# Kernel tuning notes

Hardware: AMD Instinct MI355X
Metric: run time of the kernel (lower is better)

The kernel has to match this reference:

```python
import jax, jax.numpy as jnp
import numpy as np

WS = 16          # window_size
OWS = 24         # overlap_win_size = int(ws*0.5) + ws
PAD = (OWS - WS) // 2
NH = 6           # num_heads


def _ln(x, g, b):
    m = jnp.mean(x, axis=-1, keepdims=True)
    v = jnp.mean((x - m) ** 2, axis=-1, keepdims=True)
    return (x - m) * jax.lax.rsqrt(v + 1e-5) * g + b


def setup_inputs() -> dict:
    key = jax.random.key(0)
    ks = jax.random.split(key, 12)
    B, H, W, C = 4, 64, 64, 180
    std = 0.02
    x = jax.random.normal(ks[0], (B, H * W, C), jnp.float32)
    y = jax.random.normal(ks[1], (B, H * W, C), jnp.float32)
    kv_w = jax.random.normal(ks[2], (2 * C, C), jnp.float32) * std
    kv_b = jnp.zeros((2 * C,), jnp.float32)
    q_w = jax.random.normal(ks[3], (C, C), jnp.float32) * std
    q_b = jnp.zeros((C,), jnp.float32)
    rpb = jax.random.normal(ks[4], ((WS + OWS - 1) ** 2, NH), jnp.float32) * std
    proj_w = jax.random.normal(ks[5], (C, C), jnp.float32) * std
    proj_b = jnp.zeros((C,), jnp.float32)
    fc1_w = jax.random.normal(ks[6], (4 * C, C), jnp.float32) * std
    fc1_b = jnp.zeros((4 * C,), jnp.float32)
    fc2_w = jax.random.normal(ks[7], (C, 4 * C), jnp.float32) * std
    fc2_b = jnp.zeros((C,), jnp.float32)
    norm1_g = jnp.ones((C,), jnp.float32); norm1_b = jnp.zeros((C,), jnp.float32)
    norm2_g = jnp.ones((C,), jnp.float32); norm2_b = jnp.zeros((C,), jnp.float32)
    # relative position index (HAT-style OCA): query coords vs extended window coords
    co = np.stack(np.meshgrid(np.arange(WS), np.arange(WS), indexing='ij')).reshape(2, -1)   # 2, ws*ws
    ce = np.stack(np.meshgrid(np.arange(OWS), np.arange(OWS), indexing='ij')).reshape(2, -1) # 2, ows*ows
    rel = (ce[:, None, :] - co[:, :, None]).transpose(1, 2, 0) + (WS - 1)  # nq, n, 2 in [0, ws+ows-2]
    rpi = jnp.asarray(rel[..., 0] * (WS + OWS - 1) + rel[..., 1], jnp.int32)  # [256, 576]
    return {
        'x': x, 'y': y,
        'norm1_g': norm1_g, 'norm1_b': norm1_b,
        'kv_w': kv_w, 'kv_b': kv_b, 'q_w': q_w, 'q_b': q_b,
        'rpb': rpb, 'proj_w': proj_w, 'proj_b': proj_b,
        'norm2_g': norm2_g, 'norm2_b': norm2_b,
        'fc1_w': fc1_w, 'fc1_b': fc1_b, 'fc2_w': fc2_w, 'fc2_b': fc2_b,
        'rpi': rpi, 'h': 64, 'w': 64,
    }


def reference(x, y, norm1_g, norm1_b, kv_w, kv_b, q_w, q_b, rpb, proj_w, proj_b,
              norm2_g, norm2_b, fc1_w, fc1_b, fc2_w, fc2_b, rpi, h, w):
    b, L, c = x.shape
    nh = NH
    d = c // nh
    scale = d ** -0.5
    nwh, nww = h // WS, w // WS
    nq, n = WS * WS, OWS * OWS

    shortcut = x
    xn = _ln(x, norm1_g, norm1_b).reshape(b, h, w, c)
    yn = _ln(y, norm1_g, norm1_b).reshape(b, h, w, c)

    kv = xn @ kv_w.T + kv_b                                  # b,h,w,2c
    q = yn @ q_w.T + q_b                                     # b,h,w,c

    # kv -> [2, b, c, h, w] then pad spatially and extract overlapping windows (nn.Unfold)
    kv = kv.reshape(b, h, w, 2, c).transpose(3, 0, 4, 1, 2)  # 2,b,c,h,w
    kvp = jnp.pad(kv, ((0, 0), (0, 0), (0, 0), (PAD, PAD), (PAD, PAD)))
    hh = jnp.arange(nwh)[:, None] * WS + jnp.arange(OWS)[None, :]   # [nwh, OWS]
    ww = jnp.arange(nww)[:, None] * WS + jnp.arange(OWS)[None, :]   # [nww, OWS]
    patches = kvp[:, :, :, hh][:, :, :, :, :, ww]            # 2,b,c,nwh,OWS,nww,OWS
    kvw = patches.transpose(0, 1, 3, 5, 4, 6, 2).reshape(2, b * nwh * nww, n, c)
    kwin, vwin = kvw[0], kvw[1]                              # [b_, n, c]

    # non-overlapping query windows (window_partition)
    qwin = q.reshape(b, nwh, WS, nww, WS, c).transpose(0, 1, 3, 2, 4, 5).reshape(-1, nq, c)
    b_ = qwin.shape[0]

    qh = qwin.reshape(b_, nq, nh, d).transpose(0, 2, 1, 3) * scale
    kh = kwin.reshape(b_, n, nh, d).transpose(0, 2, 1, 3)
    vh = vwin.reshape(b_, n, nh, d).transpose(0, 2, 1, 3)

    attn = jnp.einsum('bhqd,bhkd->bhqk', qh, kh)             # [b_, nh, nq, n]
    bias = rpb[rpi.reshape(-1)].reshape(nq, n, nh).transpose(2, 0, 1)  # [nh, nq, n]
    attn = jax.nn.softmax(attn + bias[None], axis=-1)
    out = jnp.einsum('bhqk,bhkd->bhqd', attn, vh).transpose(0, 2, 1, 3).reshape(b_, nq, c)

    # window_reverse
    out = out.reshape(b, nwh, nww, WS, WS, c).transpose(0, 1, 3, 2, 4, 5).reshape(b, h * w, c)

    xo = out @ proj_w.T + proj_b + shortcut
    xn2 = _ln(xo, norm2_g, norm2_b)
    mlp = jax.nn.gelu(xn2 @ fc1_w.T + fc1_b, approximate=False) @ fc2_w.T + fc2_b
    return xo + mlp
```

## Files before the change

kernel.cpp:

```cpp
#include <hip/hip_runtime.h>

typedef __bf16 bf16;
typedef __bf16 bf16x8 __attribute__((ext_vector_type(8)));
typedef __bf16 bf16x4 __attribute__((ext_vector_type(4)));
typedef __bf16 bf16x2 __attribute__((ext_vector_type(2)));
typedef float f32x4 __attribute__((ext_vector_type(4)));

static __device__ __forceinline__ bf16x8 ld8(const bf16* p) {
    return *reinterpret_cast<const bf16x8*>(p);
}
static __device__ __forceinline__ bf16x4 ld4(const bf16* p) {
    return *reinterpret_cast<const bf16x4*>(p);
}
static __device__ __forceinline__ bf16x8 ld8_b32(const bf16* p) {
    bf16x8 v;
#pragma unroll
    for (int i = 0; i < 4; ++i) {
        bf16x2 t = *reinterpret_cast<const bf16x2*>(p + i * 2);
        v[i * 2] = t[0]; v[i * 2 + 1] = t[1];
    }
    return v;
}
static __device__ __forceinline__ bf16x8 zero8() {
    bf16x8 v;
#pragma unroll
    for (int i = 0; i < 8; ++i) v[i] = (bf16)0.f;
    return v;
}

#define MFMA16(a, b, c) __builtin_amdgcn_mfma_f32_16x16x32_bf16((a), (b), (c), 0, 0, 0)

template <int ROWS, int BK, int KPAD, int THREADS>
static __device__ __forceinline__ void load_chunk_g(const bf16* __restrict__ g,
                                                    bf16x8* r, int tid) {
    constexpr int TOT = ROWS * BK / 8;
    constexpr int NP = (TOT + THREADS - 1) / THREADS;
#pragma unroll
    for (int p = 0; p < NP; ++p) {
        int idx = p * THREADS + tid;
        if ((TOT % THREADS) == 0 || idx < TOT) {
            int row = idx / (BK / 8), cg = idx % (BK / 8);
            r[p] = ld8(g + (long)row * KPAD + cg * 8);
        }
    }
}
template <int ROWS, int BK, int THREADS>
static __device__ __forceinline__ void store_chunk_l(bf16* __restrict__ lds,
                                                     const bf16x8* r, int tid) {
    constexpr int TOT = ROWS * BK / 8;
    constexpr int NP = (TOT + THREADS - 1) / THREADS;
#pragma unroll
    for (int p = 0; p < NP; ++p) {
        int idx = p * THREADS + tid;
        if ((TOT % THREADS) == 0 || idx < TOT) {
            int row = idx / (BK / 8), cg = idx % (BK / 8);
            *reinterpret_cast<bf16x8*>(lds + row * 200 + cg * 8) = r[p];
        }
    }
}
template <int ROWS, int BK, int KPAD, int THREADS>
static __device__ __forceinline__ void stage_tile(const bf16* __restrict__ g,
                                                  bf16* __restrict__ lds, int tid) {
    constexpr int TOT = ROWS * BK / 8;
    constexpr int NP = (TOT + THREADS - 1) / THREADS;
#pragma unroll
    for (int p = 0; p < NP; ++p) {
        int idx = p * THREADS + tid;
        if ((TOT % THREADS) == 0 || idx < TOT) {
            int row = idx / (BK / 8), cg = idx % (BK / 8);
            bf16x8 v = ld8(g + (long)row * KPAD + cg * 8);
            *reinterpret_cast<bf16x8*>(lds + row * 200 + cg * 8) = v;
        }
    }
}

__global__ __launch_bounds__(256) void fused_pre(
    const float* __restrict__ x, const float* __restrict__ y,
    const float* __restrict__ g, const float* __restrict__ b,
    bf16* __restrict__ dst,
    const float* __restrict__ kv_w, const float* __restrict__ q_w,
    const float* __restrict__ proj_w, const float* __restrict__ fc1_w,
    const float* __restrict__ fc2_w, const float* __restrict__ rpb,
    const int* __restrict__ rpi,
    bf16* __restrict__ wkv, bf16* __restrict__ wq, bf16* __restrict__ wproj,
    bf16* __restrict__ wfc1, bf16* __restrict__ wfc2, bf16* __restrict__ biast)
{
    if (blockIdx.x < 8192) {
        int wave = threadIdx.x >> 6, lane = threadIdx.x & 63;
        int row = blockIdx.x * 4 + wave;
        const float* sp = (row < 16384) ? (x + (long)row * 180)
                                        : (y + (long)(row - 16384) * 180);
        float v0 = sp[lane];
        float v1 = sp[lane + 64];
        float v2 = (lane < 52) ? sp[lane + 128] : 0.f;
        float s = v0 + v1 + v2;
        float sq = v0 * v0 + v1 * v1 + v2 * v2;
#pragma unroll
        for (int m = 32; m >= 1; m >>= 1) {
            s += __shfl_xor(s, m);
            sq += __shfl_xor(sq, m);
        }
        float mean = s * (1.f / 180.f);
        float var = sq * (1.f / 180.f) - mean * mean;
        float rs = rsqrtf(var + 1e-5f);
        bf16* dp = dst + (long)row * 192;
        dp[lane] = (bf16)((v0 - mean) * rs * g[lane] + b[lane]);
        dp[lane + 64] = (bf16)((v1 - mean) * rs * g[lane + 64] + b[lane + 64]);
        float o2 = (lane < 52) ? ((v2 - mean) * rs * g[lane + 128] + b[lane + 128]) : 0.f;
        dp[lane + 128] = (bf16)o2;
        return;
    }
    int i = (blockIdx.x - 8192) * 256 + threadIdx.x;
    if (i < 73728) {
        int n = i / 192, k = i % 192;
        float v = (n < 360 && k < 180) ? kv_w[n * 180 + k] : 0.f;
        wkv[i] = (bf16)v;
    } else if (i < 122880) {
        int j = i - 73728; int n = j / 192, k = j % 192;
        float v = (n < 180 && k < 180) ? q_w[n * 180 + k] : 0.f;
        wq[j] = (bf16)v;
    } else if (i < 172032) {
        int j = i - 122880; int n = j / 192, k = j % 192;
        int hh = k >> 5, d = k & 31;
        float v = (n < 180 && d < 30) ? proj_w[n * 180 + hh * 30 + d] : 0.f;
        wproj[j] = (bf16)v;
    } else if (i < 319488) {
        int j = i - 172032; int n = j / 192, k = j % 192;
        float v = (n < 720 && k < 180) ? fc1_w[n * 180 + k] : 0.f;
        wfc1[j] = (bf16)v;
    } else if (i < 507904) {
        int j = i - 319488; int n = j / 736, k = j % 736;
        float v = (n < 180 && k < 720) ? fc2_w[n * 720 + k] : 0.f;
        wfc2[j] = (bf16)v;
    } else if (i < 1392640) {
        int t = i - 507904;
        int r = t & 3;
        int lane = (t >> 2) & 63;
        int tmp2 = t >> 8;
        int kg = tmp2 % 36;
        int tmp3 = tmp2 / 36;
        int qg = tmp3 & 15;
        int h = tmp3 >> 4;
        int q = qg * 16 + (lane & 15);
        int key = kg * 16 + ((lane >> 4) << 2) + r;
        biast[t] = (bf16)rpb[rpi[q * 576 + key] * 6 + h];
    }
}

__global__ __launch_bounds__(512, 4) void gemm_kvq(
    const bf16* __restrict__ xn, const bf16* __restrict__ yn,
    const bf16* __restrict__ wkv, const bf16* __restrict__ wq,
    const float* __restrict__ kv_b, const float* __restrict__ q_b,
    bf16* __restrict__ kvbuf, bf16* __restrict__ qbuf)
{
    const int tid = threadIdx.x, wave = tid >> 6, lane = tid & 63;
    const int llo = lane & 15, quad = lane >> 4;
    const int bz = blockIdx.y;
    const bool isq = (bz == 2);
    const bf16* A = isq ? yn : xn;
    const bf16* Wbase = isq ? wq : (wkv + (long)bz * 3 * 64 * 192);
    const int tm = blockIdx.x * 128;

    __shared__ __align__(16) bf16 Sa[128 * 200];
    __shared__ __align__(16) bf16 Sb[64 * 200];

    stage_tile<128, 192, 192, 512>(A + (long)tm * 192, Sa, tid);
    bf16x8 wreg[3];
    load_chunk_g<64, 192, 192, 512>(Wbase, wreg, tid);

    for (int s = 0; s < 3; ++s) {
        if (s) __syncthreads();
        store_chunk_l<64, 192, 512>(Sb, wreg, tid);
        __syncthreads();
        if (s < 2) load_chunk_g<64, 192, 192, 512>(Wbase + (long)(s + 1) * 64 * 192, wreg, tid);

        f32x4 acc[4];
#pragma unroll
        for (int nt = 0; nt < 4; ++nt)
#pragma unroll
            for (int r = 0; r < 4; ++r) acc[nt][r] = 0.f;
#pragma unroll
        for (int kt = 0; kt < 6; ++kt) {
            bf16x8 a = ld8(Sa + (wave * 16 + llo) * 200 + kt * 32 + quad * 8);
#pragma unroll
            for (int nt = 0; nt < 4; ++nt) {
                bf16x8 b = ld8(Sb + (nt * 16 + llo) * 200 + kt * 32 + quad * 8);
                acc[nt] = MFMA16(a, b, acc[nt]);
            }
        }

        const int g = bz * 3 + s;
#pragma unroll
        for (int nt = 0; nt < 4; ++nt) {
            int n = g * 64 + nt * 16 + llo;
            if (!isq) {
                if (n < 360) {
                    int nn = n % 180;
                    int col = (n / 180) * 192 + (nn / 30) * 32 + (nn % 30);
                    float bv = kv_b[n];
#pragma unroll
                    for (int r = 0; r < 4; ++r) {
                        int m = tm + wave * 16 + quad * 4 + r;
                        kvbuf[(long)m * 384 + col] = (bf16)(acc[nt][r] + bv);
                    }
                }
            } else {
                int nq = n - 384;
                if (nq < 180) {
                    int col = (nq / 30) * 32 + (nq % 30);
                    float bv = q_b[nq];
#pragma unroll
                    for (int r = 0; r < 4; ++r) {
                        int m = tm + wave * 16 + quad * 4 + r;
                        qbuf[(long)m * 192 + col] =
                            (bf16)((acc[nt][r] + bv) * 0.18257418583505537f);
                    }
                }
            }
        }
    }
}

__global__ __launch_bounds__(512, 6) void attn_kernel(
    const bf16* __restrict__ qbuf, const bf16* __restrict__ kvbuf,
    const bf16* __restrict__ biast, bf16* __restrict__ obuf)
{
    const int qhalf = blockIdx.x & 1;
    const int head = (blockIdx.x >> 1) % 6;
    const int win = blockIdx.x / 12;
    const int bb = win / 16, wi = (win % 16) / 4, wj = win % 4;
    const int tid = threadIdx.x;
    const int wave = tid >> 6, lane = tid & 63;
    const int llo = lane & 15, quad = lane >> 4;
    const int qbase = qhalf * 128 + wave * 16;
    const int qg = qhalf * 8 + wave;

    __shared__ bf16 Kc[2][64][40];
    __shared__ bf16 Vt[2][32][74];
    __shared__ bf16 Ps[8][16][72];

    const int u = tid & 255;
    const int tloc = u >> 2, dq = u & 3;
    const bool isV = tid >= 256;
    int aa = tloc / 24, w0 = tloc % 24;

    const int q0 = qbase + llo;
    const int gr_q = bb * 4096 + (wi * 16 + (q0 >> 4)) * 64 + (wj * 16 + (q0 & 15));
    const bf16x8 qf = ld8(qbuf + (long)gr_q * 192 + head * 32 + quad * 8);
    const bf16* bbase = biast + ((long)(head * 16 + qg) * 36) * 256 + lane * 4;

    {
        int gy = wi * 16 + aa - 4, gx = wj * 16 + w0 - 4;
        bf16x8 st = zero8();
        if ((unsigned)gy < 64u && (unsigned)gx < 64u) {
            long gr = (long)(bb * 4096 + gy * 64 + gx) * 384;
            st = ld8(kvbuf + gr + (isV ? 192 : 0) + head * 32 + dq * 8);
        }
        if (!isV) {
            *reinterpret_cast<bf16x8*>(&Kc[0][tloc][dq * 8]) = st;
        } else {
#pragma unroll
            for (int j = 0; j < 8; ++j) Vt[0][dq * 8 + j][tloc] = st[j];
        }
    }
    __syncthreads();

    f32x4 o[2];
    float m_run = -1e30f, l_run = 0.f;
#pragma unroll
    for (int n2 = 0; n2 < 2; ++n2)
#pragma unroll
        for (int r = 0; r < 4; ++r) o[n2][r] = 0.f;

    for (int c = 0; c < 9; ++c) {
        const int cur = c & 1;

        bf16x8 stage;
        if (c < 8) {
            w0 += 16; aa += 2;
            if (w0 >= 24) { w0 -= 24; ++aa; }
            int gy = wi * 16 + aa - 4, gx = wj * 16 + w0 - 4;
            stage = zero8();
            if ((unsigned)gy < 64u && (unsigned)gx < 64u) {
                long gr = (long)(bb * 4096 + gy * 64 + gx) * 384;
                stage = ld8(kvbuf + gr + (isV ? 192 : 0) + head * 32 + dq * 8);
            }
        }

        f32x4 s[4];
#pragma unroll
        for (int kt = 0; kt < 4; ++kt) {
            bf16x8 kf = ld8(&Kc[cur][kt * 16 + llo][quad * 8]);
            f32x4 zc;
            zc[0] = 0.f; zc[1] = 0.f; zc[2] = 0.f; zc[3] = 0.f;
            s[kt] = MFMA16(kf, qf, zc);
        }

#pragma unroll
        for (int kt = 0; kt < 4; ++kt) {
            bf16x4 bv = ld4(bbase + (c * 4 + kt) * 256);
#pragma unroll
            for (int r = 0; r < 4; ++r) s[kt][r] += (float)bv[r];
        }

        float mx = s[0][0];
#pragma unroll
        for (int kt = 0; kt < 4; ++kt)
#pragma unroll
            for (int r = 0; r < 4; ++r) mx = fmaxf(mx, s[kt][r]);
        mx = fmaxf(mx, __shfl_xor(mx, 16));
        mx = fmaxf(mx, __shfl_xor(mx, 32));
        float m_new = fmaxf(m_run, mx);
        float alpha = __expf(m_run - m_new);
        float ls = 0.f;
#pragma unroll
        for (int kt = 0; kt < 4; ++kt)
#pragma unroll
            for (int r = 0; r < 4; ++r) {
                float p = __expf(s[kt][r] - m_new);
                s[kt][r] = p;
                ls += p;
            }
        ls += __shfl_xor(ls, 16);
        ls += __shfl_xor(ls, 32);
        l_run = l_run * alpha + ls;
        m_run = m_new;

#pragma unroll
        for (int r = 0; r < 4; ++r) {
            float a = __shfl(alpha, quad * 4 + r);
            o[0][r] *= a;
            o[1][r] *= a;
        }

#pragma unroll
        for (int kt = 0; kt < 4; ++kt) {
            bf16x4 pv;
#pragma unroll
            for (int r = 0; r < 4; ++r) pv[r] = (bf16)s[kt][r];
            *reinterpret_cast<bf16x4*>(&Ps[wave][llo][kt * 16 + quad * 4]) = pv;
        }

#pragma unroll
        for (int kt2 = 0; kt2 < 2; ++kt2) {
            bf16x8 pa = ld8(&Ps[wave][llo][kt2 * 32 + quad * 8]);
#pragma unroll
            for (int n2 = 0; n2 < 2; ++n2) {
                bf16x8 vb = ld8_b32(&Vt[cur][n2 * 16 + llo][kt2 * 32 + quad * 8]);
                o[n2] = MFMA16(pa, vb, o[n2]);
            }
        }

        if (c < 8) {
            if (!isV) {
                *reinterpret_cast<bf16x8*>(&Kc[1 - cur][tloc][dq * 8]) = stage;
            } else {
#pragma unroll
                for (int j = 0; j < 8; ++j) Vt[1 - cur][dq * 8 + j][tloc] = stage[j];
            }
            __syncthreads();
        }
    }

    float linv = 1.f / l_run;
#pragma unroll
    for (int r = 0; r < 4; ++r) {
        float li = __shfl(linv, quad * 4 + r);
        int q = qbase + quad * 4 + r;
        int gr = bb * 4096 + (wi * 16 + (q >> 4)) * 64 + (wj * 16 + (q & 15));
#pragma unroll
        for (int n2 = 0; n2 < 2; ++n2)
            obuf[(long)gr * 192 + head * 32 + n2 * 16 + llo] = (bf16)(o[n2][r] * li);
    }
}

__global__ __launch_bounds__(256, 3) void gemm_projln(
    const bf16* __restrict__ obuf, const bf16* __restrict__ wproj,
    const float* __restrict__ proj_b, const float* __restrict__ x,
    const float* __restrict__ g, const float* __restrict__ bln,
    float* __restrict__ xo, bf16* __restrict__ xn2)
{
    const int tid = threadIdx.x, wave = tid >> 6, lane = tid & 63;
    const int llo = lane & 15, quad = lane >> 4;
    const int mbase = blockIdx.x * 64;

    __shared__ __align__(16) bf16 Sa[64 * 200];
    __shared__ __align__(16) bf16 Sb[64 * 200];
    stage_tile<64, 192, 192, 256>(obuf + (long)mbase * 192, Sa, tid);
    bf16x8 wreg[6];
    load_chunk_g<64, 192, 192, 256>(wproj, wreg, tid);

    f32x4 acc[12];
#pragma unroll
    for (int nt = 0; nt < 12; ++nt)
#pragma unroll
        for (int r = 0; r < 4; ++r) acc[nt][r] = 0.f;

    for (int nc = 0; nc < 3; ++nc) {
        if (nc) __syncthreads();
        store_chunk_l<64, 192, 256>(Sb, wreg, tid);
        __syncthreads();
        if (nc < 2) load_chunk_g<64, 192, 192, 256>(wproj + (long)(nc + 1) * 64 * 192, wreg, tid);
#pragma unroll
        for (int kt = 0; kt < 6; ++kt) {
            bf16x8 a = ld8(Sa + (wave * 16 + llo) * 200 + kt * 32 + quad * 8);
#pragma unroll
            for (int nt = 0; nt < 4; ++nt) {
                bf16x8 b = ld8(Sb + (nt * 16 + llo) * 200 + kt * 32 + quad * 8);
                acc[nc * 4 + nt] = MFMA16(a, b, acc[nc * 4 + nt]);
            }
        }
    }

#pragma unroll
    for (int r = 0; r < 4; ++r) {
        int m = mbase + wave * 16 + quad * 4 + r;
        float v[12];
        float sum = 0.f, sq = 0.f;
#pragma unroll
        for (int nt = 0; nt < 12; ++nt) {
            int n = nt * 16 + llo;
            float val = 0.f;
            if (n < 180) val = acc[nt][r] + proj_b[n] + x[(long)m * 180 + n];
            v[nt] = val;
            sum += val; sq += val * val;
        }
#pragma unroll
        for (int msk = 1; msk <= 8; msk <<= 1) {
            sum += __shfl_xor(sum, msk);
            sq  += __shfl_xor(sq, msk);
        }
        float mean = sum * (1.f / 180.f);
        float var = sq * (1.f / 180.f) - mean * mean;
        float rs = rsqrtf(var + 1e-5f);
#pragma unroll
        for (int nt = 0; nt < 12; ++nt) {
            int n = nt * 16 + llo;
            if (n < 180) {
                xo[(long)m * 180 + n] = v[nt];
                xn2[(long)m * 192 + n] = (bf16)((v[nt] - mean) * rs * g[n] + bln[n]);
            } else {
                xn2[(long)m * 192 + n] = (bf16)0.f;
            }
        }
    }
}

__global__ __launch_bounds__(512, 4) void gemm_fc1(
    const bf16* __restrict__ A, const bf16* __restrict__ W,
    const float* __restrict__ bias, bf16* __restrict__ outp)
{
    const int tid = threadIdx.x, wave = tid >> 6, lane = tid & 63;
    const int llo = lane & 15, quad = lane >> 4;
    const int tm = blockIdx.x * 128;
    const int bz = blockIdx.y;
    const bf16* Wbase = W + (long)bz * 3 * 64 * 192;

    __shared__ __align__(16) bf16 Sa[128 * 200];
    __shared__ __align__(16) bf16 Sb[64 * 200];
    stage_tile<128, 192, 192, 512>(A + (long)tm * 192, Sa, tid);
    bf16x8 wreg[3];
    load_chunk_g<64, 192, 192, 512>(Wbase, wreg, tid);

    for (int s = 0; s < 3; ++s) {
        if (s) __syncthreads();
        store_chunk_l<64, 192, 512>(Sb, wreg, tid);
        __syncthreads();
        if (s < 2) load_chunk_g<64, 192, 192, 512>(Wbase + (long)(s + 1) * 64 * 192, wreg, tid);

        f32x4 acc[4];
#pragma unroll
        for (int nt = 0; nt < 4; ++nt)
#pragma unroll
            for (int r = 0; r < 4; ++r) acc[nt][r] = 0.f;
#pragma unroll
        for (int kt = 0; kt < 6; ++kt) {
            bf16x8 a = ld8(Sa + (wave * 16 + llo) * 200 + kt * 32 + quad * 8);
#pragma unroll
            for (int nt = 0; nt < 4; ++nt) {
                bf16x8 b = ld8(Sb + (nt * 16 + llo) * 200 + kt * 32 + quad * 8);
                acc[nt] = MFMA16(a, b, acc[nt]);
            }
        }

        const int nb = (bz * 3 + s) * 64;
#pragma unroll
        for (int nt = 0; nt < 4; ++nt) {
            int n = nb + nt * 16 + llo;
            if (n >= 720) continue;
            float bv = bias[n];
#pragma unroll
            for (int r = 0; r < 4; ++r) {
                int m = tm + wave * 16 + quad * 4 + r;
                float v = acc[nt][r] + bv;
                float gel = 0.5f * v * (1.f + erff(v * 0.7071067811865475f));
                outp[(long)m * 736 + n] = (bf16)gel;
            }
        }
    }
}

__global__ __launch_bounds__(256, 4) void gemm_fc2(
    const bf16* __restrict__ A, const bf16* __restrict__ W,
    const float* __restrict__ bias, const float* __restrict__ resid,
    float* __restrict__ outp)
{
    const int tid = threadIdx.x, wave = tid >> 6, lane = tid & 63;
    const int llo = lane & 15, quad = lane >> 4;
    const int tm = blockIdx.x * 64;
    const int tn = blockIdx.y * 64;

    __shared__ __align__(16) bf16 Sa[64 * 200];
    __shared__ __align__(16) bf16 Sb[64 * 200];

    const bf16* Ap = A + (long)tm * 736;
    const bf16* Wp = W + (long)tn * 736;

    bf16x8 ar[6], wr[6];
    load_chunk_g<64, 192, 736, 256>(Ap, ar, tid);
    load_chunk_g<64, 192, 736, 256>(Wp, wr, tid);

    f32x4 acc[4];
#pragma unroll
    for (int nt = 0; nt < 4; ++nt)
#pragma unroll
        for (int r = 0; r < 4; ++r) acc[nt][r] = 0.f;

#pragma unroll
    for (int c = 0; c < 4; ++c) {
        if (c) __syncthreads();
        if (c < 3) {
            store_chunk_l<64, 192, 256>(Sa, ar, tid);
            store_chunk_l<64, 192, 256>(Sb, wr, tid);
        } else {
            store_chunk_l<64, 160, 256>(Sa, ar, tid);
            store_chunk_l<64, 160, 256>(Sb, wr, tid);
        }
        __syncthreads();
        if (c < 2) {
            load_chunk_g<64, 192, 736, 256>(Ap + (c + 1) * 192, ar, tid);
            load_chunk_g<64, 192, 736, 256>(Wp + (c + 1) * 192, wr, tid);
        } else if (c == 2) {
            load_chunk_g<64, 160, 736, 256>(Ap + 576, ar, tid);
            load_chunk_g<64, 160, 736, 256>(Wp + 576, wr, tid);
        }
        const int nkt = (c == 3) ? 5 : 6;
        for (int kt = 0; kt < nkt; ++kt) {
            bf16x8 a = ld8(Sa + (wave * 16 + llo) * 200 + kt * 32 + quad * 8);
#pragma unroll
            for (int nt = 0; nt < 4; ++nt) {
                bf16x8 b = ld8(Sb + (nt * 16 + llo) * 200 + kt * 32 + quad * 8);
                acc[nt] = MFMA16(a, b, acc[nt]);
            }
        }
    }

#pragma unroll
    for (int nt = 0; nt < 4; ++nt)
#pragma unroll
        for (int r = 0; r < 4; ++r) {
            int m = tm + wave * 16 + quad * 4 + r;
            int n = tn + nt * 16 + llo;
            if (n >= 180) continue;
            float v = acc[nt][r] + bias[n];
            outp[(long)m * 180 + n] = v + resid[(long)m * 180 + n];
        }
}

extern "C" void kernel_launch(void* const* d_in, const int* in_sizes, int n_in,
                              void* d_out, int out_size, void* d_ws, size_t ws_size,
                              hipStream_t stream) {
    const float* x      = (const float*)d_in[0];
    const float* y      = (const float*)d_in[1];
    const float* n1g    = (const float*)d_in[2];
    const float* n1b    = (const float*)d_in[3];
    const float* kv_w   = (const float*)d_in[4];
    const float* kv_b   = (const float*)d_in[5];
    const float* q_w    = (const float*)d_in[6];
    const float* q_b    = (const float*)d_in[7];
    const float* rpb    = (const float*)d_in[8];
    const float* proj_w = (const float*)d_in[9];
    const float* proj_b = (const float*)d_in[10];
    const float* n2g    = (const float*)d_in[11];
    const float* n2b    = (const float*)d_in[12];
    const float* fc1_w  = (const float*)d_in[13];
    const float* fc1_b  = (const float*)d_in[14];
    const float* fc2_w  = (const float*)d_in[15];
    const float* fc2_b  = (const float*)d_in[16];
    const int*   rpi    = (const int*)d_in[17];

    char* ws = (char*)d_ws;
    bf16* xn    = (bf16*)(ws + 0);
    bf16* yn    = (bf16*)(ws + 6291456);
    bf16* qbuf  = (bf16*)(ws + 12582912);
    bf16* kvbuf = (bf16*)(ws + 18874368);
    bf16* obuf  = (bf16*)(ws + 31457280);
    float* xo   = (float*)(ws + 37748736);
    bf16* biast = (bf16*)(ws + 49545216);
    bf16* wkv   = (bf16*)(ws + 51314688);
    bf16* wq    = (bf16*)(ws + 51462144);
    bf16* wproj = (bf16*)(ws + 51560448);
    bf16* wfc1  = (bf16*)(ws + 51658752);
    bf16* wfc2  = (bf16*)(ws + 51953664);
    bf16* hmid  = (bf16*)(ws + 6291456);
    bf16* xn2   = xn;

    fused_pre<<<13632, 256, 0, stream>>>(x, y, n1g, n1b, xn,
                                         kv_w, q_w, proj_w, fc1_w, fc2_w, rpb, rpi,
                                         wkv, wq, wproj, wfc1, wfc2, biast);
    gemm_kvq<<<dim3(128, 3), 512, 0, stream>>>(xn, yn, wkv, wq, kv_b, q_b, kvbuf, qbuf);
    attn_kernel<<<768, 512, 0, stream>>>(qbuf, kvbuf, biast, obuf);
    gemm_projln<<<256, 256, 0, stream>>>(obuf, wproj, proj_b, x, n2g, n2b, xo, xn2);
    gemm_fc1<<<dim3(128, 4), 512, 0, stream>>>(xn2, wfc1, fc1_b, hmid);
    gemm_fc2<<<dim3(256, 3), 256, 0, stream>>>(hmid, wfc2, fc2_b, xo, (float*)d_out);
}
```

Baseline: 200.0 us.

## Merge all stages into one persistent kernel with grid-wide barriers

Replaces the six separate kernel launches with a single persistent kernel of 256 blocks. The stages (layernorm plus weight prep, KV/Q GEMM, windowed attention, projection plus layernorm, fc1, fc2) are separated by atomic grid barriers. Work is redistributed over a fixed block count with per-block loops, and the barrier counters are reset each call with a memset. This removes launch gaps and tail effects between stages. In exchange, occupancy is limited to 256 blocks, which may leave the GPU's compute units underused, and the barriers spin-wait and assume every block is co-resident.

```diff
diff --git a/kernel.cpp b/kernel.cpp
--- a/kernel.cpp
+++ b/kernel.cpp
@@ -74,497 +74,523 @@
     }
 }
 
-__global__ __launch_bounds__(256) void fused_pre(
+#define NBLK 256u
+
+static __device__ __forceinline__ void gridbar(unsigned* bar) {
+    __threadfence();
+    __syncthreads();
+    if (threadIdx.x == 0) {
+        __hip_atomic_fetch_add(bar, 1u, __ATOMIC_ACQ_REL, __HIP_MEMORY_SCOPE_AGENT);
+        while (__hip_atomic_load(bar, __ATOMIC_ACQUIRE, __HIP_MEMORY_SCOPE_AGENT) < NBLK)
+            __builtin_amdgcn_s_sleep(2);
+    }
+    __syncthreads();
+    __threadfence();
+}
+
+__global__ __launch_bounds__(512, 2) void mega(
     const float* __restrict__ x, const float* __restrict__ y,
-    const float* __restrict__ g, const float* __restrict__ b,
-    bf16* __restrict__ dst,
-    const float* __restrict__ kv_w, const float* __restrict__ q_w,
-    const float* __restrict__ proj_w, const float* __restrict__ fc1_w,
-    const float* __restrict__ fc2_w, const float* __restrict__ rpb,
-    const int* __restrict__ rpi,
-    bf16* __restrict__ wkv, bf16* __restrict__ wq, bf16* __restrict__ wproj,
-    bf16* __restrict__ wfc1, bf16* __restrict__ wfc2, bf16* __restrict__ biast)
+    const float* __restrict__ n1g, const float* __restrict__ n1b,
+    const float* __restrict__ kv_w, const float* __restrict__ kv_b,
+    const float* __restrict__ q_w, const float* __restrict__ q_b,
+    const float* __restrict__ rpb, const int* __restrict__ rpi,
+    const float* __restrict__ proj_w, const float* __restrict__ proj_b,
+    const float* __restrict__ n2g, const float* __restrict__ n2b,
+    const float* __restrict__ fc1_w, const float* __restrict__ fc1_b,
+    const float* __restrict__ fc2_w, const float* __restrict__ fc2_b,
+    bf16* __restrict__ xn, bf16* __restrict__ yn,
+    bf16* __restrict__ qbuf, bf16* __restrict__ kvbuf,
+    bf16* __restrict__ obuf, float* __restrict__ xo,
+    bf16* __restrict__ biast, bf16* __restrict__ wkv, bf16* __restrict__ wq,
+    bf16* __restrict__ wproj, bf16* __restrict__ wfc1, bf16* __restrict__ wfc2,
+    bf16* __restrict__ hmid, bf16* __restrict__ xn2,
+    float* __restrict__ outp, unsigned* __restrict__ bars)
 {
-    if (blockIdx.x < 8192) {
-        int wave = threadIdx.x >> 6, lane = threadIdx.x & 63;
-        int row = blockIdx.x * 4 + wave;
-        const float* sp = (row < 16384) ? (x + (long)row * 180)
-                                        : (y + (long)(row - 16384) * 180);
-        float v0 = sp[lane];
-        float v1 = sp[lane + 64];
-        float v2 = (lane < 52) ? sp[lane + 128] : 0.f;
-        float s = v0 + v1 + v2;
-        float sq = v0 * v0 + v1 * v1 + v2 * v2;
-#pragma unroll
-        for (int m = 32; m >= 1; m >>= 1) {
-            s += __shfl_xor(s, m);
-            sq += __shfl_xor(sq, m);
-        }
-        float mean = s * (1.f / 180.f);
-        float var = sq * (1.f / 180.f) - mean * mean;
-        float rs = rsqrtf(var + 1e-5f);
-        bf16* dp = dst + (long)row * 192;
-        dp[lane] = (bf16)((v0 - mean) * rs * g[lane] + b[lane]);
-        dp[lane + 64] = (bf16)((v1 - mean) * rs * g[lane + 64] + b[lane + 64]);
-        float o2 = (lane < 52) ? ((v2 - mean) * rs * g[lane + 128] + b[lane + 128]) : 0.f;
-        dp[lane + 128] = (bf16)o2;
-        return;
-    }
-    int i = (blockIdx.x - 8192) * 256 + threadIdx.x;
-    if (i < 73728) {
-        int n = i / 192, k = i % 192;
-        float v = (n < 360 && k < 180) ? kv_w[n * 180 + k] : 0.f;
-        wkv[i] = (bf16)v;
-    } else if (i < 122880) {
-        int j = i - 73728; int n = j / 192, k = j % 192;
-        float v = (n < 180 && k < 180) ? q_w[n * 180 + k] : 0.f;
-        wq[j] = (bf16)v;
-    } else if (i < 172032) {
-        int j = i - 122880; int n = j / 192, k = j % 192;
-        int hh = k >> 5, d = k & 31;
-        float v = (n < 180 && d < 30) ? proj_w[n * 180 + hh * 30 + d] : 0.f;
-        wproj[j] = (bf16)v;
-    } else if (i < 319488) {
-        int j = i - 172032; int n = j / 192, k = j % 192;
-        float v = (n < 720 && k < 180) ? fc1_w[n * 180 + k] : 0.f;
-        wfc1[j] = (bf16)v;
-    } else if (i < 507904) {
-        int j = i - 319488; int n = j / 736, k = j % 736;
-        float v = (n < 180 && k < 720) ? fc2_w[n * 720 + k] : 0.f;
-        wfc2[j] = (bf16)v;
-    } else if (i < 1392640) {
-        int t = i - 507904;
-        int r = t & 3;
-        int lane = (t >> 2) & 63;
-        int tmp2 = t >> 8;
-        int kg = tmp2 % 36;
-        int tmp3 = tmp2 / 36;
-        int qg = tmp3 & 15;
-        int h = tmp3 >> 4;
-        int q = qg * 16 + (lane & 15);
-        int key = kg * 16 + ((lane >> 4) << 2) + r;
-        biast[t] = (bf16)rpb[rpi[q * 576 + key] * 6 + h];
-    }
-}
-
-__global__ __launch_bounds__(512, 4) void gemm_kvq(
-    const bf16* __restrict__ xn, const bf16* __restrict__ yn,
-    const bf16* __restrict__ wkv, const bf16* __restrict__ wq,
-    const float* __restrict__ kv_b, const float* __restrict__ q_b,
-    bf16* __restrict__ kvbuf, bf16* __restrict__ qbuf)
-{
-    const int tid = threadIdx.x, wave = tid >> 6, lane = tid & 63;
+    __shared__ __align__(16) char SM[76800];
+    const int tid = threadIdx.x;
+    const int blk = blockIdx.x;
+    const int wave = tid >> 6, lane = tid & 63;
     const int llo = lane & 15, quad = lane >> 4;
-    const int bz = blockIdx.y;
-    const bool isq = (bz == 2);
-    const bf16* A = isq ? yn : xn;
-    const bf16* Wbase = isq ? wq : (wkv + (long)bz * 3 * 64 * 192);
-    const int tm = blockIdx.x * 128;
-
-    __shared__ __align__(16) bf16 Sa[128 * 200];
-    __shared__ __align__(16) bf16 Sb[64 * 200];
-
-    stage_tile<128, 192, 192, 512>(A + (long)tm * 192, Sa, tid);
-    bf16x8 wreg[3];
-    load_chunk_g<64, 192, 192, 512>(Wbase, wreg, tid);
-
-    for (int s = 0; s < 3; ++s) {
-        if (s) __syncthreads();
-        store_chunk_l<64, 192, 512>(Sb, wreg, tid);
+
+    {
+#pragma unroll 2
+        for (int it = 0; it < 16; ++it) {
+            int row = blk * 128 + it * 8 + wave;
+            const float* sp = (row < 16384) ? (x + (long)row * 180)
+                                            : (y + (long)(row - 16384) * 180);
+            float v0 = sp[lane];
+            float v1 = sp[lane + 64];
+            float v2 = (lane < 52) ? sp[lane + 128] : 0.f;
+            float s = v0 + v1 + v2;
+            float sq = v0 * v0 + v1 * v1 + v2 * v2;
+#pragma unroll
+            for (int m = 32; m >= 1; m >>= 1) {
+                s += __shfl_xor(s, m);
+                sq += __shfl_xor(sq, m);
+            }
+            float mean = s * (1.f / 180.f);
+            float var = sq * (1.f / 180.f) - mean * mean;
+            float rs = rsqrtf(var + 1e-5f);
+            bf16* dp = ((row < 16384) ? xn : (yn - 16384 * 192)) + (long)row * 192;
+            dp[lane] = (bf16)((v0 - mean) * rs * n1g[lane] + n1b[lane]);
+            dp[lane + 64] = (bf16)((v1 - mean) * rs * n1g[lane + 64] + n1b[lane + 64]);
+            float o2 = (lane < 52) ? ((v2 - mean) * rs * n1g[lane + 128] + n1b[lane + 128]) : 0.f;
+            dp[lane + 128] = (bf16)o2;
+        }
+        for (int i = blk * 512 + tid; i < 1392640; i += 131072) {
+            if (i < 73728) {
+                int n = i / 192, k = i % 192;
+                float v = (n < 360 && k < 180) ? kv_w[n * 180 + k] : 0.f;
+                wkv[i] = (bf16)v;
+            } else if (i < 122880) {
+                int j = i - 73728; int n = j / 192, k = j % 192;
+                float v = (n < 180 && k < 180) ? q_w[n * 180 + k] : 0.f;
+                wq[j] = (bf16)v;
+            } else if (i < 172032) {
+                int j = i - 122880; int n = j / 192, k = j % 192;
+                int hh = k >> 5, d = k & 31;
+                float v = (n < 180 && d < 30) ? proj_w[n * 180 + hh * 30 + d] : 0.f;
+                wproj[j] = (bf16)v;
+            } else if (i < 319488) {
+                int j = i - 172032; int n = j / 192, k = j % 192;
+                float v = (n < 720 && k < 180) ? fc1_w[n * 180 + k] : 0.f;
+                wfc1[j] = (bf16)v;
+            } else if (i < 507904) {
+                int j = i - 319488; int n = j / 736, k = j % 736;
+                float v = (n < 180 && k < 720) ? fc2_w[n * 720 + k] : 0.f;
+                wfc2[j] = (bf16)v;
+            } else {
+                int t = i - 507904;
+                int r = t & 3;
+                int ln = (t >> 2) & 63;
+                int tmp2 = t >> 8;
+                int kg = tmp2 % 36;
+                int tmp3 = tmp2 / 36;
+                int qg = tmp3 & 15;
+                int h = tmp3 >> 4;
+                int q = qg * 16 + (ln & 15);
+                int key = kg * 16 + ((ln >> 4) << 2) + r;
+                biast[t] = (bf16)rpb[rpi[q * 576 + key] * 6 + h];
+            }
+        }
+    }
+    gridbar(bars + 0);
+
+    {
+        bf16* Sa = (bf16*)SM;
+        bf16* Sb = (bf16*)(SM + 51200);
+        const int tmi = blk >> 1;
+        const int tm = tmi * 128;
+        const bool oddb = blk & 1;
+        const bf16* A = oddb ? yn : xn;
+        stage_tile<128, 192, 192, 512>(A + (long)tm * 192, Sa, tid);
+        const int nbz = oddb ? 1 : 2;
+        for (int zz = 0; zz < nbz; ++zz) {
+            const int bz = oddb ? 2 : zz;
+            const bool isq = (bz == 2);
+            const bf16* Wbase = isq ? wq : (wkv + (long)bz * 3 * 64 * 192);
+            bf16x8 wreg[3];
+            load_chunk_g<64, 192, 192, 512>(Wbase, wreg, tid);
+            for (int s = 0; s < 3; ++s) {
+                if (s || zz) __syncthreads();
+                store_chunk_l<64, 192, 512>(Sb, wreg, tid);
+                __syncthreads();
+                if (s < 2) load_chunk_g<64, 192, 192, 512>(Wbase + (long)(s + 1) * 64 * 192, wreg, tid);
+
+                f32x4 acc[4];
+#pragma unroll
+                for (int nt = 0; nt < 4; ++nt)
+#pragma unroll
+                    for (int r = 0; r < 4; ++r) acc[nt][r] = 0.f;
+#pragma unroll
+                for (int kt = 0; kt < 6; ++kt) {
+                    bf16x8 a = ld8(Sa + (wave * 16 + llo) * 200 + kt * 32 + quad * 8);
+#pragma unroll
+                    for (int nt = 0; nt < 4; ++nt) {
+                        bf16x8 b = ld8(Sb + (nt * 16 + llo) * 200 + kt * 32 + quad * 8);
+                        acc[nt] = MFMA16(a, b, acc[nt]);
+                    }
+                }
+
+                const int g = bz * 3 + s;
+#pragma unroll
+                for (int nt = 0; nt < 4; ++nt) {
+                    int n = g * 64 + nt * 16 + llo;
+                    if (!isq) {
+                        if (n < 360) {
+                            int nn = n % 180;
+                            int col = (n / 180) * 192 + (nn / 30) * 32 + (nn % 30);
+                            float bv = kv_b[n];
+#pragma unroll
+                            for (int r = 0; r < 4; ++r) {
+                                int m = tm + wave * 16 + quad * 4 + r;
+                                kvbuf[(long)m * 384 + col] = (bf16)(acc[nt][r] + bv);
+                            }
+                        }
+                    } else {
+                        int nq = n - 384;
+                        if (nq < 180) {
+                            int col = (nq / 30) * 32 + (nq % 30);
+                            float bv = q_b[nq];
+#pragma unroll
+                            for (int r = 0; r < 4; ++r) {
+                                int m = tm + wave * 16 + quad * 4 + r;
+                                qbuf[(long)m * 192 + col] =
+                                    (bf16)((acc[nt][r] + bv) * 0.18257418583505537f);
+                            }
+                        }
+                    }
+                }
+            }
+        }
+    }
+    gridbar(bars + 1);
+
+    {
+        bf16 (*Kc)[64][40] = reinterpret_cast<bf16 (*)[64][40]>(SM);
+        bf16 (*Vt)[32][74] = reinterpret_cast<bf16 (*)[32][74]>(SM + 10240);
+        bf16 (*Ps)[16][72] = reinterpret_cast<bf16 (*)[16][72]>(SM + 19712);
+
+        for (int tt = 0; tt < 3; ++tt) {
+            if (tt) __syncthreads();
+            const int t = blk * 3 + tt;
+            const int win = t / 12, sub = t % 12;
+            const int qhalf = sub & 1, head = sub >> 1;
+            const int bb = win / 16, wi = (win % 16) / 4, wj = win % 4;
+            const int qbase = qhalf * 128 + wave * 16;
+            const int qg = qhalf * 8 + wave;
+
+            const int u = tid & 255;
+            const int tloc = u >> 2, dq = u & 3;
+            const bool isV = tid >= 256;
+            int aa = tloc / 24, w0 = tloc % 24;
+
+            const int q0 = qbase + llo;
+            const int gr_q = bb * 4096 + (wi * 16 + (q0 >> 4)) * 64 + (wj * 16 + (q0 & 15));
+            const bf16x8 qf = ld8(qbuf + (long)gr_q * 192 + head * 32 + quad * 8);
+            const bf16* bbase = biast + ((long)(head * 16 + qg) * 36) * 256 + lane * 4;
+
+            {
+                int gy = wi * 16 + aa - 4, gx = wj * 16 + w0 - 4;
+                bf16x8 st = zero8();
+                if ((unsigned)gy < 64u && (unsigned)gx < 64u) {
+                    long gr = (long)(bb * 4096 + gy * 64 + gx) * 384;
+                    st = ld8(kvbuf + gr + (isV ? 192 : 0) + head * 32 + dq * 8);
+                }
+                if (!isV) {
+                    *reinterpret_cast<bf16x8*>(&Kc[0][tloc][dq * 8]) = st;
+                } else {
+#pragma unroll
+                    for (int j = 0; j < 8; ++j) Vt[0][dq * 8 + j][tloc] = st[j];
+                }
+            }
+            __syncthreads();
+
+            f32x4 o[2];
+            float m_run = -1e30f, l_run = 0.f;
+#pragma unroll
+            for (int n2 = 0; n2 < 2; ++n2)
+#pragma unroll
+                for (int r = 0; r < 4; ++r) o[n2][r] = 0.f;
+
+            for (int c = 0; c < 9; ++c) {
+                const int cur = c & 1;
+
+                bf16x8 stage;
+                if (c < 8) {
+                    w0 += 16; aa += 2;
+                    if (w0 >= 24) { w0 -= 24; ++aa; }
+                    int gy = wi * 16 + aa - 4, gx = wj * 16 + w0 - 4;
+                    stage = zero8();
+                    if ((unsigned)gy < 64u && (unsigned)gx < 64u) {
+                        long gr = (long)(bb * 4096 + gy * 64 + gx) * 384;
+                        stage = ld8(kvbuf + gr + (isV ? 192 : 0) + head * 32 + dq * 8);
+                    }
+                }
+
+                f32x4 s[4];
+#pragma unroll
+                for (int kt = 0; kt < 4; ++kt) {
+                    bf16x8 kf = ld8(&Kc[cur][kt * 16 + llo][quad * 8]);
+                    f32x4 zc;
+                    zc[0] = 0.f; zc[1] = 0.f; zc[2] = 0.f; zc[3] = 0.f;
+                    s[kt] = MFMA16(kf, qf, zc);
+                }
+
+#pragma unroll
+                for (int kt = 0; kt < 4; ++kt) {
+                    bf16x4 bv = ld4(bbase + (c * 4 + kt) * 256);
+#pragma unroll
+                    for (int r = 0; r < 4; ++r) s[kt][r] += (float)bv[r];
+                }
+
+                float mx = s[0][0];
+#pragma unroll
+                for (int kt = 0; kt < 4; ++kt)
+#pragma unroll
+                    for (int r = 0; r < 4; ++r) mx = fmaxf(mx, s[kt][r]);
+                mx = fmaxf(mx, __shfl_xor(mx, 16));
+                mx = fmaxf(mx, __shfl_xor(mx, 32));
+                float m_new = fmaxf(m_run, mx);
+                float alpha = __expf(m_run - m_new);
+                float ls = 0.f;
+#pragma unroll
+                for (int kt = 0; kt < 4; ++kt)
+#pragma unroll
+                    for (int r = 0; r < 4; ++r) {
+                        float p = __expf(s[kt][r] - m_new);
+                        s[kt][r] = p;
+                        ls += p;
+                    }
+                ls += __shfl_xor(ls, 16);
+                ls += __shfl_xor(ls, 32);
+                l_run = l_run * alpha + ls;
+                m_run = m_new;
+
+#pragma unroll
+                for (int r = 0; r < 4; ++r) {
+                    float a = __shfl(alpha, quad * 4 + r);
+                    o[0][r] *= a;
+                    o[1][r] *= a;
+                }
+
+#pragma unroll
+                for (int kt = 0; kt < 4; ++kt) {
+                    bf16x4 pv;
+#pragma unroll
+                    for (int r = 0; r < 4; ++r) pv[r] = (bf16)s[kt][r];
+                    *reinterpret_cast<bf16x4*>(&Ps[wave][llo][kt * 16 + quad * 4]) = pv;
+                }
+
+#pragma unroll
+                for (int kt2 = 0; kt2 < 2; ++kt2) {
+                    bf16x8 pa = ld8(&Ps[wave][llo][kt2 * 32 + quad * 8]);
+#pragma unroll
+                    for (int n2 = 0; n2 < 2; ++n2) {
+                        bf16x8 vb = ld8_b32(&Vt[cur][n2 * 16 + llo][kt2 * 32 + quad * 8]);
+                        o[n2] = MFMA16(pa, vb, o[n2]);
+                    }
+                }
+
+                if (c < 8) {
+                    if (!isV) {
+                        *reinterpret_cast<bf16x8*>(&Kc[1 - cur][tloc][dq * 8]) = stage;
+                    } else {
+#pragma unroll
+                        for (int j = 0; j < 8; ++j) Vt[1 - cur][dq * 8 + j][tloc] = stage[j];
+                    }
+                    __syncthreads();
+                }
+            }
+
+            float linv = 1.f / l_run;
+#pragma unroll
+            for (int r = 0; r < 4; ++r) {
+                float li = __shfl(linv, quad * 4 + r);
+                int q = qbase + quad * 4 + r;
+                int gr = bb * 4096 + (wi * 16 + (q >> 4)) * 64 + (wj * 16 + (q & 15));
+#pragma unroll
+                for (int n2 = 0; n2 < 2; ++n2)
+                    obuf[(long)gr * 192 + head * 32 + n2 * 16 + llo] = (bf16)(o[n2][r] * li);
+            }
+        }
+    }
+    gridbar(bars + 2);
+
+    {
+        bf16* Sa = (bf16*)SM;
+        bf16* Sb = (bf16*)(SM + 25600);
+        float* Pr = (float*)(SM + 64000);
+        const int rt = wave >> 1, ch = wave & 1;
+        const int mbase = blk * 64;
+
+        stage_tile<64, 192, 192, 512>(obuf + (long)mbase * 192, Sa, tid);
+        bf16x8 wreg[5];
+        load_chunk_g<96, 192, 192, 512>(wproj, wreg, tid);
+
+        f32x4 acc[6];
+#pragma unroll
+        for (int t6 = 0; t6 < 6; ++t6)
+#pragma unroll
+            for (int r = 0; r < 4; ++r) acc[t6][r] = 0.f;
+
+        for (int nc = 0; nc < 2; ++nc) {
+            if (nc) __syncthreads();
+            store_chunk_l<96, 192, 512>(Sb, wreg, tid);
+            __syncthreads();
+            if (nc == 0) load_chunk_g<96, 192, 192, 512>(wproj + 96L * 192, wreg, tid);
+#pragma unroll
+            for (int kt = 0; kt < 6; ++kt) {
+                bf16x8 a = ld8(Sa + (rt * 16 + llo) * 200 + kt * 32 + quad * 8);
+#pragma unroll
+                for (int ctl = 0; ctl < 3; ++ctl) {
+                    bf16x8 b = ld8(Sb + (ch * 48 + ctl * 16 + llo) * 200 + kt * 32 + quad * 8);
+                    acc[nc * 3 + ctl] = MFMA16(a, b, acc[nc * 3 + ctl]);
+                }
+            }
+        }
+
+        float v[4][6];
+#pragma unroll
+        for (int r = 0; r < 4; ++r) {
+            float sum = 0.f, sq = 0.f;
+#pragma unroll
+            for (int t6 = 0; t6 < 6; ++t6) {
+                int n = (t6 / 3) * 96 + ch * 48 + (t6 % 3) * 16 + llo;
+                float val = 0.f;
+                if (n < 180) {
+                    int m = mbase + rt * 16 + quad * 4 + r;
+                    val = acc[t6][r] + proj_b[n] + x[(long)m * 180 + n];
+                }
+                v[r][t6] = val;
+                sum += val; sq += val * val;
+            }
+#pragma unroll
+            for (int msk = 1; msk <= 8; msk <<= 1) {
+                sum += __shfl_xor(sum, msk);
+                sq  += __shfl_xor(sq, msk);
+            }
+            if (llo == 0) {
+                int rl = rt * 16 + quad * 4 + r;
+                Pr[rl * 4 + ch * 2] = sum;
+                Pr[rl * 4 + ch * 2 + 1] = sq;
+            }
+        }
         __syncthreads();
-        if (s < 2) load_chunk_g<64, 192, 192, 512>(Wbase + (long)(s + 1) * 64 * 192, wreg, tid);
-
-        f32x4 acc[4];
-#pragma unroll
-        for (int nt = 0; nt < 4; ++nt)
-#pragma unroll
-            for (int r = 0; r < 4; ++r) acc[nt][r] = 0.f;
-#pragma unroll
-        for (int kt = 0; kt < 6; ++kt) {
-            bf16x8 a = ld8(Sa + (wave * 16 + llo) * 200 + kt * 32 + quad * 8);
-#pragma unroll
-            for (int nt = 0; nt < 4; ++nt) {
-                bf16x8 b = ld8(Sb + (nt * 16 + llo) * 200 + kt * 32 + quad * 8);
-                acc[nt] = MFMA16(a, b, acc[nt]);
-            }
-        }
-
-        const int g = bz * 3 + s;
-#pragma unroll
-        for (int nt = 0; nt < 4; ++nt) {
-            int n = g * 64 + nt * 16 + llo;
-            if (!isq) {
-                if (n < 360) {
-                    int nn = n % 180;
-                    int col = (n / 180) * 192 + (nn / 30) * 32 + (nn % 30);
-                    float bv = kv_b[n];
+#pragma unroll
+        for (int r = 0; r < 4; ++r) {
+            int rl = rt * 16 + quad * 4 + r;
+            float sum = Pr[rl * 4] + Pr[rl * 4 + 2];
+            float sq  = Pr[rl * 4 + 1] + Pr[rl * 4 + 3];
+            float mean = sum * (1.f / 180.f);
+            float var = sq * (1.f / 180.f) - mean * mean;
+            float rs = rsqrtf(var + 1e-5f);
+            int m = mbase + rl;
+#pragma unroll
+            for (int t6 = 0; t6 < 6; ++t6) {
+                int n = (t6 / 3) * 96 + ch * 48 + (t6 % 3) * 16 + llo;
+                if (n < 180) {
+                    xo[(long)m * 180 + n] = v[r][t6];
+                    xn2[(long)m * 192 + n] = (bf16)((v[r][t6] - mean) * rs * n2g[n] + n2b[n]);
+                } else {
+                    xn2[(long)m * 192 + n] = (bf16)0.f;
+                }
+            }
+        }
+    }
+    gridbar(bars + 3);
+
+    {
+        bf16* Sa = (bf16*)SM;
+        bf16* Sb = (bf16*)(SM + 51200);
+        const int tmi = blk >> 1;
+        const int tm = tmi * 128;
+        stage_tile<128, 192, 192, 512>(xn2 + (long)tm * 192, Sa, tid);
+        for (int zz = 0; zz < 2; ++zz) {
+            const int bz = (blk & 1) * 2 + zz;
+            const bf16* Wbase = wfc1 + (long)bz * 3 * 64 * 192;
+            bf16x8 wreg[3];
+            load_chunk_g<64, 192, 192, 512>(Wbase, wreg, tid);
+            for (int s = 0; s < 3; ++s) {
+                if (s || zz) __syncthreads();
+                store_chunk_l<64, 192, 512>(Sb, wreg, tid);
+                __syncthreads();
+                if (s < 2) load_chunk_g<64, 192, 192, 512>(Wbase + (long)(s + 1) * 64 * 192, wreg, tid);
+
+                f32x4 acc[4];
+#pragma unroll
+                for (int nt = 0; nt < 4; ++nt)
+#pragma unroll
+                    for (int r = 0; r < 4; ++r) acc[nt][r] = 0.f;
+#pragma unroll
+                for (int kt = 0; kt < 6; ++kt) {
+                    bf16x8 a = ld8(Sa + (wave * 16 + llo) * 200 + kt * 32 + quad * 8);
+#pragma unroll
+                    for (int nt = 0; nt < 4; ++nt) {
+                        bf16x8 b = ld8(Sb + (nt * 16 + llo) * 200 + kt * 32 + quad * 8);
+                        acc[nt] = MFMA16(a, b, acc[nt]);
+                    }
+                }
+
+                const int nb = (bz * 3 + s) * 64;
+#pragma unroll
+                for (int nt = 0; nt < 4; ++nt) {
+                    int n = nb + nt * 16 + llo;
+                    if (n >= 720) continue;
+                    float bv = fc1_b[n];
 #pragma unroll
                     for (int r = 0; r < 4; ++r) {
                         int m = tm + wave * 16 + quad * 4 + r;
-                        kvbuf[(long)m * 384 + col] = (bf16)(acc[nt][r] + bv);
-                    }
-                }
-            } else {
-                int nq = n - 384;
-                if (nq < 180) {
-                    int col = (nq / 30) * 32 + (nq % 30);
-                    float bv = q_b[nq];
-#pragma unroll
-                    for (int r = 0; r < 4; ++r) {
-                        int m = tm + wave * 16 + quad * 4 + r;
-                        qbuf[(long)m * 192 + col] =
-                            (bf16)((acc[nt][r] + bv) * 0.18257418583505537f);
-                    }
-                }
-            }
-        }
-    }
-}
-
-__global__ __launch_bounds__(512, 6) void attn_kernel(
-    const bf16* __restrict__ qbuf, const bf16* __restrict__ kvbuf,
-    const bf16* __restrict__ biast, bf16* __restrict__ obuf)
-{
-    const int qhalf = blockIdx.x & 1;
-    const int head = (blockIdx.x >> 1) % 6;
-    const int win = blockIdx.x / 12;
-    const int bb = win / 16, wi = (win % 16) / 4, wj = win % 4;
-    const int tid = threadIdx.x;
-    const int wave = tid >> 6, lane = tid & 63;
-    const int llo = lane & 15, quad = lane >> 4;
-    const int qbase = qhalf * 128 + wave * 16;
-    const int qg = qhalf * 8 + wave;
-
-    __shared__ bf16 Kc[2][64][40];
-    __shared__ bf16 Vt[2][32][74];
-    __shared__ bf16 Ps[8][16][72];
-
-    const int u = tid & 255;
-    const int tloc = u >> 2, dq = u & 3;
-    const bool isV = tid >= 256;
-    int aa = tloc / 24, w0 = tloc % 24;
-
-    const int q0 = qbase + llo;
-    const int gr_q = bb * 4096 + (wi * 16 + (q0 >> 4)) * 64 + (wj * 16 + (q0 & 15));
-    const bf16x8 qf = ld8(qbuf + (long)gr_q * 192 + head * 32 + quad * 8);
-    const bf16* bbase = biast + ((long)(head * 16 + qg) * 36) * 256 + lane * 4;
+                        float vv = acc[nt][r] + bv;
+                        float gel = 0.5f * vv * (1.f + erff(vv * 0.7071067811865475f));
+                        hmid[(long)m * 736 + n] = (bf16)gel;
+                    }
+                }
+            }
+        }
+    }
+    gridbar(bars + 4);
 
     {
-        int gy = wi * 16 + aa - 4, gx = wj * 16 + w0 - 4;
-        bf16x8 st = zero8();
-        if ((unsigned)gy < 64u && (unsigned)gx < 64u) {
-            long gr = (long)(bb * 4096 + gy * 64 + gx) * 384;
-            st = ld8(kvbuf + gr + (isV ? 192 : 0) + head * 32 + dq * 8);
-        }
-        if (!isV) {
-            *reinterpret_cast<bf16x8*>(&Kc[0][tloc][dq * 8]) = st;
-        } else {
-#pragma unroll
-            for (int j = 0; j < 8; ++j) Vt[0][dq * 8 + j][tloc] = st[j];
-        }
-    }
-    __syncthreads();
-
-    f32x4 o[2];
-    float m_run = -1e30f, l_run = 0.f;
-#pragma unroll
-    for (int n2 = 0; n2 < 2; ++n2)
-#pragma unroll
-        for (int r = 0; r < 4; ++r) o[n2][r] = 0.f;
-
-    for (int c = 0; c < 9; ++c) {
-        const int cur = c & 1;
-
-        bf16x8 stage;
-        if (c < 8) {
-            w0 += 16; aa += 2;
-            if (w0 >= 24) { w0 -= 24; ++aa; }
-            int gy = wi * 16 + aa - 4, gx = wj * 16 + w0 - 4;
-            stage = zero8();
-            if ((unsigned)gy < 64u && (unsigned)gx < 64u) {
-                long gr = (long)(bb * 4096 + gy * 64 + gx) * 384;
-                stage = ld8(kvbuf + gr + (isV ? 192 : 0) + head * 32 + dq * 8);
-            }
-        }
-
-        f32x4 s[4];
-#pragma unroll
-        for (int kt = 0; kt < 4; ++kt) {
-            bf16x8 kf = ld8(&Kc[cur][kt * 16 + llo][quad * 8]);
-            f32x4 zc;
-            zc[0] = 0.f; zc[1] = 0.f; zc[2] = 0.f; zc[3] = 0.f;
-            s[kt] = MFMA16(kf, qf, zc);
-        }
-
-#pragma unroll
-        for (int kt = 0; kt < 4; ++kt) {
-            bf16x4 bv = ld4(bbase + (c * 4 + kt) * 256);
-#pragma unroll
-            for (int r = 0; r < 4; ++r) s[kt][r] += (float)bv[r];
-        }
-
-        float mx = s[0][0];
-#pragma unroll
-        for (int kt = 0; kt < 4; ++kt)
-#pragma unroll
-            for (int r = 0; r < 4; ++r) mx = fmaxf(mx, s[kt][r]);
-        mx = fmaxf(mx, __shfl_xor(mx, 16));
-        mx = fmaxf(mx, __shfl_xor(mx, 32));
-        float m_new = fmaxf(m_run, mx);
-        float alpha = __expf(m_run - m_new);
-        float ls = 0.f;
-#pragma unroll
-        for (int kt = 0; kt < 4; ++kt)
-#pragma unroll
-            for (int r = 0; r < 4; ++r) {
-                float p = __expf(s[kt][r] - m_new);
-                s[kt][r] = p;
-                ls += p;
-            }
-        ls += __shfl_xor(ls, 16);
-        ls += __shfl_xor(ls, 32);
-        l_run = l_run * alpha + ls;
-        m_run = m_new;
-
-#pragma unroll
-        for (int r = 0; r < 4; ++r) {
-            float a = __shfl(alpha, quad * 4 + r);
-            o[0][r] *= a;
-            o[1][r] *= a;
-        }
-
-#pragma unroll
-        for (int kt = 0; kt < 4; ++kt) {
-            bf16x4 pv;
-#pragma unroll
-            for (int r = 0; r < 4; ++r) pv[r] = (bf16)s[kt][r];
-            *reinterpret_cast<bf16x4*>(&Ps[wave][llo][kt * 16 + quad * 4]) = pv;
-        }
-
-#pragma unroll
-        for (int kt2 = 0; kt2 < 2; ++kt2) {
-            bf16x8 pa = ld8(&Ps[wave][llo][kt2 * 32 + quad * 8]);
-#pragma unroll
-            for (int n2 = 0; n2 < 2; ++n2) {
-                bf16x8 vb = ld8_b32(&Vt[cur][n2 * 16 + llo][kt2 * 32 + quad * 8]);
-                o[n2] = MFMA16(pa, vb, o[n2]);
-            }
-        }
-
-        if (c < 8) {
-            if (!isV) {
-                *reinterpret_cast<bf16x8*>(&Kc[1 - cur][tloc][dq * 8]) = stage;
-            } else {
-#pragma unroll
-                for (int j = 0; j < 8; ++j) Vt[1 - cur][dq * 8 + j][tloc] = stage[j];
-            }
-            __syncthreads();
-        }
-    }
-
-    float linv = 1.f / l_run;
-#pragma unroll
-    for (int r = 0; r < 4; ++r) {
-        float li = __shfl(linv, quad * 4 + r);
-        int q = qbase + quad * 4 + r;
-        int gr = bb * 4096 + (wi * 16 + (q >> 4)) * 64 + (wj * 16 + (q & 15));
-#pragma unroll
-        for (int n2 = 0; n2 < 2; ++n2)
-            obuf[(long)gr * 192 + head * 32 + n2 * 16 + llo] = (bf16)(o[n2][r] * li);
-    }
-}
-
-__global__ __launch_bounds__(256, 3) void gemm_projln(
-    const bf16* __restrict__ obuf, const bf16* __restrict__ wproj,
-    const float* __restrict__ proj_b, const float* __restrict__ x,
-    const float* __restrict__ g, const float* __restrict__ bln,
-    float* __restrict__ xo, bf16* __restrict__ xn2)
-{
-    const int tid = threadIdx.x, wave = tid >> 6, lane = tid & 63;
-    const int llo = lane & 15, quad = lane >> 4;
-    const int mbase = blockIdx.x * 64;
-
-    __shared__ __align__(16) bf16 Sa[64 * 200];
-    __shared__ __align__(16) bf16 Sb[64 * 200];
-    stage_tile<64, 192, 192, 256>(obuf + (long)mbase * 192, Sa, tid);
-    bf16x8 wreg[6];
-    load_chunk_g<64, 192, 192, 256>(wproj, wreg, tid);
-
-    f32x4 acc[12];
-#pragma unroll
-    for (int nt = 0; nt < 12; ++nt)
-#pragma unroll
-        for (int r = 0; r < 4; ++r) acc[nt][r] = 0.f;
-
-    for (int nc = 0; nc < 3; ++nc) {
-        if (nc) __syncthreads();
-        store_chunk_l<64, 192, 256>(Sb, wreg, tid);
-        __syncthreads();
-        if (nc < 2) load_chunk_g<64, 192, 192, 256>(wproj + (long)(nc + 1) * 64 * 192, wreg, tid);
-#pragma unroll
-        for (int kt = 0; kt < 6; ++kt) {
-            bf16x8 a = ld8(Sa + (wave * 16 + llo) * 200 + kt * 32 + quad * 8);
-#pragma unroll
-            for (int nt = 0; nt < 4; ++nt) {
-                bf16x8 b = ld8(Sb + (nt * 16 + llo) * 200 + kt * 32 + quad * 8);
-                acc[nc * 4 + nt] = MFMA16(a, b, acc[nc * 4 + nt]);
-            }
-        }
-    }
-
-#pragma unroll
-    for (int r = 0; r < 4; ++r) {
-        int m = mbase + wave * 16 + quad * 4 + r;
-        float v[12];
-        float sum = 0.f, sq = 0.f;
-#pragma unroll
-        for (int nt = 0; nt < 12; ++nt) {
-            int n = nt * 16 + llo;
-            float val = 0.f;
-            if (n < 180) val = acc[nt][r] + proj_b[n] + x[(long)m * 180 + n];
-            v[nt] = val;
-            sum += val; sq += val * val;
-        }
-#pragma unroll
-        for (int msk = 1; msk <= 8; msk <<= 1) {
-            sum += __shfl_xor(sum, msk);
-            sq  += __shfl_xor(sq, msk);
-        }
-        float mean = sum * (1.f / 180.f);
-        float var = sq * (1.f / 180.f) - mean * mean;
-        float rs = rsqrtf(var + 1e-5f);
-#pragma unroll
-        for (int nt = 0; nt < 12; ++nt) {
-            int n = nt * 16 + llo;
-            if (n < 180) {
-                xo[(long)m * 180 + n] = v[nt];
-                xn2[(long)m * 192 + n] = (bf16)((v[nt] - mean) * rs * g[n] + bln[n]);
-            } else {
-                xn2[(long)m * 192 + n] = (bf16)0.f;
-            }
-        }
-    }
-}
-
-__global__ __launch_bounds__(512, 4) void gemm_fc1(
-    const bf16* __restrict__ A, const bf16* __restrict__ W,
-    const float* __restrict__ bias, bf16* __restrict__ outp)
-{
-    const int tid = threadIdx.x, wave = tid >> 6, lane = tid & 63;
-    const int llo = lane & 15, quad = lane >> 4;
-    const int tm = blockIdx.x * 128;
-    const int bz = blockIdx.y;
-    const bf16* Wbase = W + (long)bz * 3 * 64 * 192;
-
-    __shared__ __align__(16) bf16 Sa[128 * 200];
-    __shared__ __align__(16) bf16 Sb[64 * 200];
-    stage_tile<128, 192, 192, 512>(A + (long)tm * 192, Sa, tid);
-    bf16x8 wreg[3];
-    load_chunk_g<64, 192, 192, 512>(Wbase, wreg, tid);
-
-    for (int s = 0; s < 3; ++s) {
-        if (s) __syncthreads();
-        store_chunk_l<64, 192, 512>(Sb, wreg, tid);
-        __syncthreads();
-        if (s < 2) load_chunk_g<64, 192, 192, 512>(Wbase + (long)(s + 1) * 64 * 192, wreg, tid);
-
-        f32x4 acc[4];
-#pragma unroll
-        for (int nt = 0; nt < 4; ++nt)
-#pragma unroll
-            for (int r = 0; r < 4; ++r) acc[nt][r] = 0.f;
-#pragma unroll
-        for (int kt = 0; kt < 6; ++kt) {
-            bf16x8 a = ld8(Sa + (wave * 16 + llo) * 200 + kt * 32 + quad * 8);
-#pragma unroll
-            for (int nt = 0; nt < 4; ++nt) {
-                bf16x8 b = ld8(Sb + (nt * 16 + llo) * 200 + kt * 32 + quad * 8);
-                acc[nt] = MFMA16(a, b, acc[nt]);
-            }
-        }
-
-        const int nb = (bz * 3 + s) * 64;
-#pragma unroll
-        for (int nt = 0; nt < 4; ++nt) {
-            int n = nb + nt * 16 + llo;
-            if (n >= 720) continue;
-            float bv = bias[n];
-#pragma unroll
-            for (int r = 0; r < 4; ++r) {
-                int m = tm + wave * 16 + quad * 4 + r;
-                float v = acc[nt][r] + bv;
-                float gel = 0.5f * v * (1.f + erff(v * 0.7071067811865475f));
-                outp[(long)m * 736 + n] = (bf16)gel;
-            }
-        }
-    }
-}
-
-__global__ __launch_bounds__(256, 4) void gemm_fc2(
-    const bf16* __restrict__ A, const bf16* __restrict__ W,
-    const float* __restrict__ bias, const float* __restrict__ resid,
-    float* __restrict__ outp)
-{
-    const int tid = threadIdx.x, wave = tid >> 6, lane = tid & 63;
-    const int llo = lane & 15, quad = lane >> 4;
-    const int tm = blockIdx.x * 64;
-    const int tn = blockIdx.y * 64;
-
-    __shared__ __align__(16) bf16 Sa[64 * 200];
-    __shared__ __align__(16) bf16 Sb[64 * 200];
-
-    const bf16* Ap = A + (long)tm * 736;
-    const bf16* Wp = W + (long)tn * 736;
-
-    bf16x8 ar[6], wr[6];
-    load_chunk_g<64, 192, 736, 256>(Ap, ar, tid);
-    load_chunk_g<64, 192, 736, 256>(Wp, wr, tid);
-
-    f32x4 acc[4];
-#pragma unroll
-    for (int nt = 0; nt < 4; ++nt)
-#pragma unroll
-        for (int r = 0; r < 4; ++r) acc[nt][r] = 0.f;
-
-#pragma unroll
-    for (int c = 0; c < 4; ++c) {
-        if (c) __syncthreads();
-        if (c < 3) {
-            store_chunk_l<64, 192, 256>(Sa, ar, tid);
-            store_chunk_l<64, 192, 256>(Sb, wr, tid);
-        } else {
-            store_chunk_l<64, 160, 256>(Sa, ar, tid);
-            store_chunk_l<64, 160, 256>(Sb, wr, tid);
-        }
-        __syncthreads();
-        if (c < 2) {
-            load_chunk_g<64, 192, 736, 256>(Ap + (c + 1) * 192, ar, tid);
-            load_chunk_g<64, 192, 736, 256>(Wp + (c + 1) * 192, wr, tid);
-        } else if (c == 2) {
-            load_chunk_g<64, 160, 736, 256>(Ap + 576, ar, tid);
-            load_chunk_g<64, 160, 736, 256>(Wp + 576, wr, tid);
-        }
-        const int nkt = (c == 3) ? 5 : 6;
-        for (int kt = 0; kt < nkt; ++kt) {
-            bf16x8 a = ld8(Sa + (wave * 16 + llo) * 200 + kt * 32 + quad * 8);
-#pragma unroll
-            for (int nt = 0; nt < 4; ++nt) {
-                bf16x8 b = ld8(Sb + (nt * 16 + llo) * 200 + kt * 32 + quad * 8);
-                acc[nt] = MFMA16(a, b, acc[nt]);
-            }
-        }
-    }
-
-#pragma unroll
-    for (int nt = 0; nt < 4; ++nt)
-#pragma unroll
-        for (int r = 0; r < 4; ++r) {
-            int m = tm + wave * 16 + quad * 4 + r;
-            int n = tn + nt * 16 + llo;
-            if (n >= 180) continue;
-            float v = acc[nt][r] + bias[n];
-            outp[(long)m * 180 + n] = v + resid[(long)m * 180 + n];
-        }
+        bf16* Sa = (bf16*)SM;
+        bf16* Sb = (bf16*)(SM + 25600);
+        const int rt = wave >> 1, chn = wave & 1;
+        const int tm = blk * 64;
+        const bf16* Ap = hmid + (long)tm * 736;
+        for (int tni = 0; tni < 3; ++tni) {
+            const int tn = tni * 64;
+            const bf16* Wp = wfc2 + (long)tn * 736;
+            bf16x8 ar[3], wr[3];
+            load_chunk_g<64, 192, 736, 512>(Ap, ar, tid);
+            load_chunk_g<64, 192, 736, 512>(Wp, wr, tid);
+
+            f32x4 acc[2];
+#pragma unroll
+            for (int j = 0; j < 2; ++j)
+#pragma unroll
+                for (int r = 0; r < 4; ++r) acc[j][r] = 0.f;
+
+#pragma unroll
+            for (int c = 0; c < 4; ++c) {
+                if (c || tni) __syncthreads();
+                if (c < 3) {
+                    store_chunk_l<64, 192, 512>(Sa, ar, tid);
+                    store_chunk_l<64, 192, 512>(Sb, wr, tid);
+                } else {
+                    store_chunk_l<64, 160, 512>(Sa, ar, tid);
+                    store_chunk_l<64, 160, 512>(Sb, wr, tid);
+                }
+                __syncthreads();
+                if (c < 2) {
+                    load_chunk_g<64, 192, 736, 512>(Ap + (c + 1) * 192, ar, tid);
+                    load_chunk_g<64, 192, 736, 512>(Wp + (c + 1) * 192, wr, tid);
+                } else if (c == 2) {
+                    load_chunk_g<64, 160, 736, 512>(Ap + 576, ar, tid);
+                    load_chunk_g<64, 160, 736, 512>(Wp + 576, wr, tid);
+                }
+                const int nkt = (c == 3) ? 5 : 6;
+                for (int kt = 0; kt < nkt; ++kt) {
+                    bf16x8 a = ld8(Sa + (rt * 16 + llo) * 200 + kt * 32 + quad * 8);
+#pragma unroll
+                    for (int j = 0; j < 2; ++j) {
+                        bf16x8 b = ld8(Sb + ((chn * 2 + j) * 16 + llo) * 200 + kt * 32 + quad * 8);
+                        acc[j] = MFMA16(a, b, acc[j]);
+                    }
+                }
+            }
+
+#pragma unroll
+            for (int j = 0; j < 2; ++j)
+#pragma unroll
+                for (int r = 0; r < 4; ++r) {
+                    int m = tm + rt * 16 + quad * 4 + r;
+                    int n = tn + (chn * 2 + j) * 16 + llo;
+                    if (n >= 180) continue;
+                    float vv = acc[j][r] + fc2_b[n];
+                    outp[(long)m * 180 + n] = vv + xo[(long)m * 180 + n];
+                }
+        }
+    }
 }
 
 extern "C" void kernel_launch(void* const* d_in, const int* in_sizes, int n_in,
@@ -604,13 +630,12 @@
     bf16* wfc2  = (bf16*)(ws + 51953664);
     bf16* hmid  = (bf16*)(ws + 6291456);
     bf16* xn2   = xn;
-
-    fused_pre<<<13632, 256, 0, stream>>>(x, y, n1g, n1b, xn,
-                                         kv_w, q_w, proj_w, fc1_w, fc2_w, rpb, rpi,
-                                         wkv, wq, wproj, wfc1, wfc2, biast);
-    gemm_kvq<<<dim3(128, 3), 512, 0, stream>>>(xn, yn, wkv, wq, kv_b, q_b, kvbuf, qbuf);
-    attn_kernel<<<768, 512, 0, stream>>>(qbuf, kvbuf, biast, obuf);
-    gemm_projln<<<256, 256, 0, stream>>>(obuf, wproj, proj_b, x, n2g, n2b, xo, xn2);
-    gemm_fc1<<<dim3(128, 4), 512, 0, stream>>>(xn2, wfc1, fc1_b, hmid);
-    gemm_fc2<<<dim3(256, 3), 256, 0, stream>>>(hmid, wfc2, fc2_b, xo, (float*)d_out);
-}
+    unsigned* bars = (unsigned*)(ws + 52428800);
+
+    hipMemsetAsync(ws + 52428800, 0, 64, stream);
+    mega<<<NBLK, 512, 0, stream>>>(x, y, n1g, n1b, kv_w, kv_b, q_w, q_b, rpb, rpi,
+                                   proj_w, proj_b, n2g, n2b, fc1_w, fc1_b, fc2_w, fc2_b,
+                                   xn, yn, qbuf, kvbuf, obuf, xo, biast,
+                                   wkv, wq, wproj, wfc1, wfc2, hmid, xn2,
+                                   (float*)d_out, bars);
+}
```

Result: slower. 704.4 us (+252.2%).
